# Optimization experiments

Hardware: AMD Instinct MI355X
Metric: run time of the kernel (lower is better)

## Reference

```python
import jax, jax.numpy as jnp
import numpy as np

B, T, N, K, d = 16, 64, 256, 8, 8
D = K * d
NEG = -9e15  # matches torch's -9000000000000000.0 sentinel


def _xavier(key, out_dim, in_dim):
    lim = float(np.sqrt(6.0 / (in_dim + out_dim)))
    return jax.random.uniform(key, (out_dim, in_dim), jnp.float32, -lim, lim)


def setup_inputs() -> dict:
    key = jax.random.key(0)
    ks = jax.random.split(key, 12)
    X = jax.random.normal(ks[0], (B, T, N, D), jnp.float32)
    STE = jax.random.normal(ks[1], (B, T, N, D), jnp.float32)
    W12 = _xavier(ks[2], D, 2 * D); b12 = jnp.zeros((D,), jnp.float32)
    W13 = _xavier(ks[3], D, 2 * D); b13 = jnp.zeros((D,), jnp.float32)
    W14 = _xavier(ks[4], D, 2 * D); b14 = jnp.zeros((D,), jnp.float32)
    W15 = _xavier(ks[5], D, D);     b15 = jnp.zeros((D,), jnp.float32)
    W16 = _xavier(ks[6], D, D);     b16 = jnp.zeros((D,), jnp.float32)
    return dict(X=X, STE=STE, W12=W12, b12=b12, W13=W13, b13=b13,
                W14=W14, b14=b14, W15=W15, b15=b15, W16=W16, b16=b16)


def reference(X, STE, W12, b12, W13, b13, W14, b14, W15, b15, W16, b16):
    gelu = lambda x: jax.nn.gelu(x, approximate=False)  # torch F.gelu default = erf
    Bv, Tv, Nv, Dv = X.shape
    H = jnp.concatenate([X, STE], axis=-1)              # [B,T,N,2D]
    # GELU-activated QKV projections, split into K heads of width d on last dim
    q = gelu(H @ W12.T + b12).reshape(Bv, Tv, Nv, K, d)
    k = gelu(H @ W13.T + b13).reshape(Bv, Tv, Nv, K, d)
    v = gelu(H @ W14.T + b14).reshape(Bv, Tv, Nv, K, d)
    # attention over time axis per (batch, vertex, head)
    attn = jnp.einsum('bqnkd,bsnkd->bnkqs', q, k) / jnp.sqrt(jnp.float32(d))
    causal = jnp.tril(jnp.ones((Tv, Tv), bool))         # [T,T]
    attn = jnp.where(causal, attn, jnp.float32(NEG))
    attn = jax.nn.softmax(attn, axis=-1)
    out = jnp.einsum('bnkqs,bsnkd->bqnkd', attn, v).reshape(Bv, Tv, Nv, Dv)
    # output MLP (dropout is identity in eval)
    return gelu(out @ W15.T + b15) @ W16.T + b16
```

## Files before the change

### kernel.cpp

```cpp
#include <hip/hip_runtime.h>
#include <hip/hip_bf16.h>

#define Bn 16
#define Tn 64
#define Nn 256
#define Kn 8
#define dn 8
#define Dn 64
#define TDn 128

typedef __bf16 bf16x8 __attribute__((ext_vector_type(8)));
typedef __bf16 bf16x4 __attribute__((ext_vector_type(4)));
typedef __bf16 bf16x2 __attribute__((ext_vector_type(2)));
typedef float  f32x4  __attribute__((ext_vector_type(4)));

#if __has_builtin(__builtin_amdgcn_exp2f)
#define EXP2F(x) __builtin_amdgcn_exp2f(x)
#else
#define EXP2F(x) exp2f(x)
#endif

#if __has_builtin(__builtin_amdgcn_rcpf)
#define RCPF(x) __builtin_amdgcn_rcpf(x)
#else
#define RCPF(x) (1.0f / (x))
#endif

__device__ __forceinline__ float geluf(float x) {
    const float x2 = x * x;
    const float v = x * fmaf(0.10294342f, x2, 2.30220920f);
    const float w = EXP2F(-fabsf(v));
    const float r = RCPF(1.0f + w);
    const float t = (1.0f - w) * r;
    return fmaf(0.5f * fabsf(x), t, 0.5f * x);
}

__device__ __forceinline__ bf16x8 bzero8() {
    bf16x8 z;
    #pragma unroll
    for (int e = 0; e < 8; ++e) z[e] = (__bf16)0.0f;
    return z;
}
__device__ __forceinline__ bf16x4 bzero4() {
    bf16x4 z;
    #pragma unroll
    for (int e = 0; e < 4; ++e) z[e] = (__bf16)0.0f;
    return z;
}

__global__ void convert_weights(const float* __restrict__ W12, const float* __restrict__ W13,
                                const float* __restrict__ W14, const float* __restrict__ W15,
                                const float* __restrict__ W16, __bf16* __restrict__ ws)
{
    const int i = blockIdx.x * 256 + threadIdx.x;
    float v;
    if      (i < 8192)  v = W12[i];
    else if (i < 16384) v = W13[i - 8192];
    else if (i < 24576) v = W14[i - 16384];
    else if (i < 28672) v = W15[i - 24576];
    else                v = W16[i - 28672];
    ws[i] = (__bf16)v;
}

template <int J>
__device__ __forceinline__ void attn_tile(__bf16 (*qs)[72], __bf16 (*Ps)[40],
                                          bf16x8 kf0, bf16x8 kf1, bf16x8 kf2, bf16x8 kf3,
                                          bf16x8 vf0, bf16x8 vf1,
                                          int hc, int cl, int quad, int kb)
{
    bf16x8 qf = bzero8();
    if (quad == 0) qf = *reinterpret_cast<const bf16x8*>(&qs[16 * J + cl][hc]);

    const f32x4 zc = {0.f, 0.f, 0.f, 0.f};
    f32x4 st[4];
    st[0] = __builtin_amdgcn_mfma_f32_16x16x32_bf16(kf0, qf, zc, 0, 0, 0);
    if constexpr (J >= 1) st[1] = __builtin_amdgcn_mfma_f32_16x16x32_bf16(kf1, qf, zc, 0, 0, 0);
    if constexpr (J >= 2) st[2] = __builtin_amdgcn_mfma_f32_16x16x32_bf16(kf2, qf, zc, 0, 0, 0);
    if constexpr (J >= 3) st[3] = __builtin_amdgcn_mfma_f32_16x16x32_bf16(kf3, qf, zc, 0, 0, 0);

    #pragma unroll
    for (int r = 0; r < 4; ++r)
        st[J][r] = (4 * quad + r > cl) ? -3.0e38f : st[J][r];

    float mx = -3.0e38f;
    #pragma unroll
    for (int i = 0; i <= J; ++i) {
        #pragma unroll
        for (int r = 0; r < 4; ++r) mx = fmaxf(mx, st[i][r]);
    }
    mx = fmaxf(mx, __shfl_xor(mx, 16));
    mx = fmaxf(mx, __shfl_xor(mx, 32));

    float sum = 0.f;
    #pragma unroll
    for (int i = 0; i <= J; ++i) {
        #pragma unroll
        for (int r = 0; r < 4; ++r) {
            const float p = EXP2F(st[i][r] - mx);
            st[i][r] = p;
            sum += p;
        }
    }
    sum += __shfl_xor(sum, 16);
    sum += __shfl_xor(sum, 32);

    f32x4 o = {0.f, 0.f, 0.f, 0.f};

    {
        bf16x4 pk0;
        #pragma unroll
        for (int r = 0; r < 4; ++r) pk0[r] = (__bf16)st[0][r];
        *reinterpret_cast<bf16x4*>(&Ps[cl][4 * quad]) = pk0;
        if constexpr (J >= 1) {
            bf16x4 pk1;
            #pragma unroll
            for (int r = 0; r < 4; ++r) pk1[r] = (__bf16)st[1][r];
            *reinterpret_cast<bf16x4*>(&Ps[cl][16 + 4 * quad]) = pk1;
        } else {
            *reinterpret_cast<bf16x4*>(&Ps[cl][16 + 4 * quad]) = bzero4();
        }
        const bf16x8 pf = *reinterpret_cast<const bf16x8*>(&Ps[cl][kb]);
        o = __builtin_amdgcn_mfma_f32_16x16x32_bf16(vf0, pf, o, 0, 0, 0);
    }
    if constexpr (J >= 2) {
        bf16x4 pk2;
        #pragma unroll
        for (int r = 0; r < 4; ++r) pk2[r] = (__bf16)st[2][r];
        *reinterpret_cast<bf16x4*>(&Ps[cl][4 * quad]) = pk2;
        if constexpr (J >= 3) {
            bf16x4 pk3;
            #pragma unroll
            for (int r = 0; r < 4; ++r) pk3[r] = (__bf16)st[3][r];
            *reinterpret_cast<bf16x4*>(&Ps[cl][16 + 4 * quad]) = pk3;
        } else {
            *reinterpret_cast<bf16x4*>(&Ps[cl][16 + 4 * quad]) = bzero4();
        }
        const bf16x8 pf = *reinterpret_cast<const bf16x8*>(&Ps[cl][kb]);
        o = __builtin_amdgcn_mfma_f32_16x16x32_bf16(vf1, pf, o, 0, 0, 0);
    }

    const float inv = RCPF(sum);
    if (quad < 2) {
        bf16x4 ov;
        #pragma unroll
        for (int r = 0; r < 4; ++r) ov[r] = (__bf16)(o[r] * inv);
        *reinterpret_cast<bf16x4*>(&qs[16 * J + cl][hc + 4 * quad]) = ov;
    }
}

__global__ __launch_bounds__(256, 5)
void tam_fused(const float* __restrict__ X,
               const float* __restrict__ STE,
               const float* __restrict__ b12, const float* __restrict__ b13,
               const float* __restrict__ b14, const float* __restrict__ b15,
               const float* __restrict__ b16,
               const __bf16* __restrict__ Wb,
               float* __restrict__ Out)
{
    __shared__ __align__(16) char smem[32768];
    __bf16 (*vt)[72] = reinterpret_cast<__bf16 (*)[72]>(smem);
    __bf16 (*qs)[72] = reinterpret_cast<__bf16 (*)[72]>(smem + 9216);
    __bf16 (*ks)[72] = reinterpret_cast<__bf16 (*)[72]>(smem + 18432);

    const int bn   = blockIdx.x;
    const int b    = bn >> 8;
    const int n    = bn & 255;
    const int tid  = threadIdx.x;
    const int lane = tid & 63;
    const int wv   = __builtin_amdgcn_readfirstlane(tid >> 6);
    const int cl   = lane & 15;
    const int quad = lane >> 4;
    const int kb   = quad * 8;
    const int m0   = wv * 16;

    __bf16 (*Ps)[40] = reinterpret_cast<__bf16 (*)[40]>(smem + 27648 + wv * 1280);

    const __bf16* Wqkv = Wb;
    const __bf16* W15b = Wb + 24576;
    const __bf16* W16b = Wb + 28672;

    {
        bf16x8 af[4];
        {
            const int t = m0 + cl;
            const size_t rb = (((size_t)b * Tn + t) * Nn + n) * (size_t)Dn;
            const float4* Xr = reinterpret_cast<const float4*>(X + rb);
            const float4* Sr = reinterpret_cast<const float4*>(STE + rb);
            #pragma unroll
            for (int kk = 0; kk < 4; ++kk) {
                const float4* src = (kk < 2) ? Xr : Sr;
                const int fi = (kk & 1) * 8 + quad * 2;
                const float4 f0 = src[fi];
                const float4 f1 = src[fi + 1];
                bf16x8 a;
                a[0] = (__bf16)f0.x; a[1] = (__bf16)f0.y;
                a[2] = (__bf16)f0.z; a[3] = (__bf16)f0.w;
                a[4] = (__bf16)f1.x; a[5] = (__bf16)f1.y;
                a[6] = (__bf16)f1.z; a[7] = (__bf16)f1.w;
                af[kk] = a;
            }
        }

        #pragma unroll
        for (int nt = 0; nt < 12; ++nt) {
            const int n0 = nt * 16;
            f32x4 acc = {0.f, 0.f, 0.f, 0.f};
            if (nt < 8) {
                #pragma unroll
                for (int kk = 0; kk < 4; ++kk) {
                    const bf16x8 bf = *reinterpret_cast<const bf16x8*>(
                        &Wqkv[(n0 + cl) * TDn + kk * 32 + kb]);
                    acc = __builtin_amdgcn_mfma_f32_16x16x32_bf16(bf, af[kk], acc, 0, 0, 0);
                }
                if (nt < 4) {
                    const float4 bs = *reinterpret_cast<const float4*>(&b12[n0 + 4 * quad]);
                    bf16x4 pk;
                    pk[0] = (__bf16)(geluf(acc[0] + bs.x) * 0.51006951f);
                    pk[1] = (__bf16)(geluf(acc[1] + bs.y) * 0.51006951f);
                    pk[2] = (__bf16)(geluf(acc[2] + bs.z) * 0.51006951f);
                    pk[3] = (__bf16)(geluf(acc[3] + bs.w) * 0.51006951f);
                    *reinterpret_cast<bf16x4*>(&qs[m0 + cl][n0 + 4 * quad]) = pk;
                } else {
                    const float4 bs = *reinterpret_cast<const float4*>(&b13[n0 - 64 + 4 * quad]);
                    bf16x4 pk;
                    pk[0] = (__bf16)geluf(acc[0] + bs.x);
                    pk[1] = (__bf16)geluf(acc[1] + bs.y);
                    pk[2] = (__bf16)geluf(acc[2] + bs.z);
                    pk[3] = (__bf16)geluf(acc[3] + bs.w);
                    *reinterpret_cast<bf16x4*>(&ks[m0 + cl][n0 - 64 + 4 * quad]) = pk;
                }
            } else {
                #pragma unroll
                for (int kk = 0; kk < 4; ++kk) {
                    const bf16x8 bf = *reinterpret_cast<const bf16x8*>(
                        &Wqkv[(n0 + cl) * TDn + kk * 32 + kb]);
                    acc = __builtin_amdgcn_mfma_f32_16x16x32_bf16(af[kk], bf, acc, 0, 0, 0);
                }
                const float bias = b14[n0 - 128 + cl];
                bf16x4 pv;
                #pragma unroll
                for (int r = 0; r < 4; ++r) pv[r] = (__bf16)geluf(acc[r] + bias);
                *reinterpret_cast<bf16x4*>(&vt[n0 - 128 + cl][m0 + 4 * quad]) = pv;
            }
        }
    }
    __syncthreads();

    {
        #pragma unroll
        for (int hh = 0; hh < 2; ++hh) {
            const int h  = 2 * wv + hh;
            const int hc = 8 * h;

            bf16x8 kf0 = bzero8(), kf1 = bzero8(), kf2 = bzero8(), kf3 = bzero8();
            if (quad == 0) {
                kf0 = *reinterpret_cast<const bf16x8*>(&ks[ 0 + cl][hc]);
                kf1 = *reinterpret_cast<const bf16x8*>(&ks[16 + cl][hc]);
                kf2 = *reinterpret_cast<const bf16x8*>(&ks[32 + cl][hc]);
                kf3 = *reinterpret_cast<const bf16x8*>(&ks[48 + cl][hc]);
            }
            bf16x8 vf0 = bzero8(), vf1 = bzero8();
            if (cl < 8) {
                vf0 = *reinterpret_cast<const bf16x8*>(&vt[hc + cl][kb]);
                vf1 = *reinterpret_cast<const bf16x8*>(&vt[hc + cl][32 + kb]);
            }

            attn_tile<0>(qs, Ps, kf0, kf1, kf2, kf3, vf0, vf1, hc, cl, quad, kb);
            attn_tile<1>(qs, Ps, kf0, kf1, kf2, kf3, vf0, vf1, hc, cl, quad, kb);
            attn_tile<2>(qs, Ps, kf0, kf1, kf2, kf3, vf0, vf1, hc, cl, quad, kb);
            attn_tile<3>(qs, Ps, kf0, kf1, kf2, kf3, vf0, vf1, hc, cl, quad, kb);
        }
    }
    __syncthreads();

    {
        const bf16x8 h0 = *reinterpret_cast<const bf16x8*>(&qs[m0 + cl][kb]);
        const bf16x8 h1 = *reinterpret_cast<const bf16x8*>(&qs[m0 + cl][32 + kb]);
        #pragma unroll
        for (int nt = 0; nt < 4; ++nt) {
            const int n0 = nt * 16;
            f32x4 acc = {0.f, 0.f, 0.f, 0.f};
            const bf16x8 w0 = *reinterpret_cast<const bf16x8*>(&W15b[(n0 + cl) * Dn + kb]);
            acc = __builtin_amdgcn_mfma_f32_16x16x32_bf16(w0, h0, acc, 0, 0, 0);
            const bf16x8 w1 = *reinterpret_cast<const bf16x8*>(&W15b[(n0 + cl) * Dn + 32 + kb]);
            acc = __builtin_amdgcn_mfma_f32_16x16x32_bf16(w1, h1, acc, 0, 0, 0);
            const float4 bs = *reinterpret_cast<const float4*>(&b15[n0 + 4 * quad]);
            bf16x4 pk;
            pk[0] = (__bf16)geluf(acc[0] + bs.x);
            pk[1] = (__bf16)geluf(acc[1] + bs.y);
            pk[2] = (__bf16)geluf(acc[2] + bs.z);
            pk[3] = (__bf16)geluf(acc[3] + bs.w);
            *reinterpret_cast<bf16x4*>(&ks[m0 + cl][n0 + 4 * quad]) = pk;
        }
    }

    {
        const bf16x8 h0 = *reinterpret_cast<const bf16x8*>(&ks[m0 + cl][kb]);
        const bf16x8 h1 = *reinterpret_cast<const bf16x8*>(&ks[m0 + cl][32 + kb]);
        const size_t ob = (((size_t)(b * Tn + m0 + cl)) * Nn + n) * (size_t)Dn;
        #pragma unroll
        for (int nt = 0; nt < 4; ++nt) {
            const int n0 = nt * 16;
            f32x4 acc = {0.f, 0.f, 0.f, 0.f};
            const bf16x8 w0 = *reinterpret_cast<const bf16x8*>(&W16b[(n0 + cl) * Dn + kb]);
            acc = __builtin_amdgcn_mfma_f32_16x16x32_bf16(w0, h0, acc, 0, 0, 0);
            const bf16x8 w1 = *reinterpret_cast<const bf16x8*>(&W16b[(n0 + cl) * Dn + 32 + kb]);
            acc = __builtin_amdgcn_mfma_f32_16x16x32_bf16(w1, h1, acc, 0, 0, 0);
            const float4 bs = *reinterpret_cast<const float4*>(&b16[n0 + 4 * quad]);
            float4 ov;
            ov.x = acc[0] + bs.x;
            ov.y = acc[1] + bs.y;
            ov.z = acc[2] + bs.z;
            ov.w = acc[3] + bs.w;
            *reinterpret_cast<float4*>(&Out[ob + n0 + 4 * quad]) = ov;
        }
    }
}

extern "C" void kernel_launch(void* const* d_in, const int* in_sizes, int n_in,
                              void* d_out, int out_size, void* d_ws, size_t ws_size,
                              hipStream_t stream)
{
    (void)in_sizes; (void)n_in; (void)out_size; (void)ws_size;
    const float* X   = (const float*)d_in[0];
    const float* STE = (const float*)d_in[1];
    const float* W12 = (const float*)d_in[2];
    const float* b12 = (const float*)d_in[3];
    const float* W13 = (const float*)d_in[4];
    const float* b13 = (const float*)d_in[5];
    const float* W14 = (const float*)d_in[6];
    const float* b14 = (const float*)d_in[7];
    const float* W15 = (const float*)d_in[8];
    const float* b15 = (const float*)d_in[9];
    const float* W16 = (const float*)d_in[10];
    const float* b16 = (const float*)d_in[11];
    float* Out = (float*)d_out;
    __bf16* ws = (__bf16*)d_ws;

    hipLaunchKernelGGL(convert_weights, dim3(128), dim3(256), 0, stream,
                       W12, W13, W14, W15, W16, ws);
    hipLaunchKernelGGL(tam_fused, dim3(Bn * Nn), dim3(256), 0, stream,
                       X, STE, b12, b13, b14, b15, b16, ws, Out);
}
```

Baseline: 282.0 us.

## Rewrite causal attention with 32x32 MFMA tiles and register shuffles for P

Replaces the four 16x16 query-tile attention steps with two 32x32x16 MFMA query tiles per head. The softmax probabilities are repacked into the B operand with cross-half lane shuffles instead of round-tripping through per-wave LDS scratch, which shrinks shared memory. The aim is fewer MFMA issues, no LDS traffic for P, and possibly higher occupancy. The cost is more registers for 16-wide accumulators and more wasted work on masked causal entries within the larger tiles.

```diff
diff --git a/kernel.cpp b/kernel.cpp
--- a/kernel.cpp
+++ b/kernel.cpp
@@ -13,6 +13,7 @@
 typedef __bf16 bf16x4 __attribute__((ext_vector_type(4)));
 typedef __bf16 bf16x2 __attribute__((ext_vector_type(2)));
 typedef float  f32x4  __attribute__((ext_vector_type(4)));
+typedef float  f32x16 __attribute__((ext_vector_type(16)));
 
 #if __has_builtin(__builtin_amdgcn_exp2f)
 #define EXP2F(x) __builtin_amdgcn_exp2f(x)
@@ -39,12 +40,6 @@
     bf16x8 z;
     #pragma unroll
     for (int e = 0; e < 8; ++e) z[e] = (__bf16)0.0f;
-    return z;
-}
-__device__ __forceinline__ bf16x4 bzero4() {
-    bf16x4 z;
-    #pragma unroll
-    for (int e = 0; e < 4; ++e) z[e] = (__bf16)0.0f;
     return z;
 }
 
@@ -62,92 +57,6 @@
     ws[i] = (__bf16)v;
 }
 
-template <int J>
-__device__ __forceinline__ void attn_tile(__bf16 (*qs)[72], __bf16 (*Ps)[40],
-                                          bf16x8 kf0, bf16x8 kf1, bf16x8 kf2, bf16x8 kf3,
-                                          bf16x8 vf0, bf16x8 vf1,
-                                          int hc, int cl, int quad, int kb)
-{
-    bf16x8 qf = bzero8();
-    if (quad == 0) qf = *reinterpret_cast<const bf16x8*>(&qs[16 * J + cl][hc]);
-
-    const f32x4 zc = {0.f, 0.f, 0.f, 0.f};
-    f32x4 st[4];
-    st[0] = __builtin_amdgcn_mfma_f32_16x16x32_bf16(kf0, qf, zc, 0, 0, 0);
-    if constexpr (J >= 1) st[1] = __builtin_amdgcn_mfma_f32_16x16x32_bf16(kf1, qf, zc, 0, 0, 0);
-    if constexpr (J >= 2) st[2] = __builtin_amdgcn_mfma_f32_16x16x32_bf16(kf2, qf, zc, 0, 0, 0);
-    if constexpr (J >= 3) st[3] = __builtin_amdgcn_mfma_f32_16x16x32_bf16(kf3, qf, zc, 0, 0, 0);
-
-    #pragma unroll
-    for (int r = 0; r < 4; ++r)
-        st[J][r] = (4 * quad + r > cl) ? -3.0e38f : st[J][r];
-
-    float mx = -3.0e38f;
-    #pragma unroll
-    for (int i = 0; i <= J; ++i) {
-        #pragma unroll
-        for (int r = 0; r < 4; ++r) mx = fmaxf(mx, st[i][r]);
-    }
-    mx = fmaxf(mx, __shfl_xor(mx, 16));
-    mx = fmaxf(mx, __shfl_xor(mx, 32));
-
-    float sum = 0.f;
-    #pragma unroll
-    for (int i = 0; i <= J; ++i) {
-        #pragma unroll
-        for (int r = 0; r < 4; ++r) {
-            const float p = EXP2F(st[i][r] - mx);
-            st[i][r] = p;
-            sum += p;
-        }
-    }
-    sum += __shfl_xor(sum, 16);
-    sum += __shfl_xor(sum, 32);
-
-    f32x4 o = {0.f, 0.f, 0.f, 0.f};
-
-    {
-        bf16x4 pk0;
-        #pragma unroll
-        for (int r = 0; r < 4; ++r) pk0[r] = (__bf16)st[0][r];
-        *reinterpret_cast<bf16x4*>(&Ps[cl][4 * quad]) = pk0;
-        if constexpr (J >= 1) {
-            bf16x4 pk1;
-            #pragma unroll
-            for (int r = 0; r < 4; ++r) pk1[r] = (__bf16)st[1][r];
-            *reinterpret_cast<bf16x4*>(&Ps[cl][16 + 4 * quad]) = pk1;
-        } else {
-            *reinterpret_cast<bf16x4*>(&Ps[cl][16 + 4 * quad]) = bzero4();
-        }
-        const bf16x8 pf = *reinterpret_cast<const bf16x8*>(&Ps[cl][kb]);
-        o = __builtin_amdgcn_mfma_f32_16x16x32_bf16(vf0, pf, o, 0, 0, 0);
-    }
-    if constexpr (J >= 2) {
-        bf16x4 pk2;
-        #pragma unroll
-        for (int r = 0; r < 4; ++r) pk2[r] = (__bf16)st[2][r];
-        *reinterpret_cast<bf16x4*>(&Ps[cl][4 * quad]) = pk2;
-        if constexpr (J >= 3) {
-            bf16x4 pk3;
-            #pragma unroll
-            for (int r = 0; r < 4; ++r) pk3[r] = (__bf16)st[3][r];
-            *reinterpret_cast<bf16x4*>(&Ps[cl][16 + 4 * quad]) = pk3;
-        } else {
-            *reinterpret_cast<bf16x4*>(&Ps[cl][16 + 4 * quad]) = bzero4();
-        }
-        const bf16x8 pf = *reinterpret_cast<const bf16x8*>(&Ps[cl][kb]);
-        o = __builtin_amdgcn_mfma_f32_16x16x32_bf16(vf1, pf, o, 0, 0, 0);
-    }
-
-    const float inv = RCPF(sum);
-    if (quad < 2) {
-        bf16x4 ov;
-        #pragma unroll
-        for (int r = 0; r < 4; ++r) ov[r] = (__bf16)(o[r] * inv);
-        *reinterpret_cast<bf16x4*>(&qs[16 * J + cl][hc + 4 * quad]) = ov;
-    }
-}
-
 __global__ __launch_bounds__(256, 5)
 void tam_fused(const float* __restrict__ X,
                const float* __restrict__ STE,
@@ -157,7 +66,7 @@
                const __bf16* __restrict__ Wb,
                float* __restrict__ Out)
 {
-    __shared__ __align__(16) char smem[32768];
+    __shared__ __align__(16) char smem[27648];
     __bf16 (*vt)[72] = reinterpret_cast<__bf16 (*)[72]>(smem);
     __bf16 (*qs)[72] = reinterpret_cast<__bf16 (*)[72]>(smem + 9216);
     __bf16 (*ks)[72] = reinterpret_cast<__bf16 (*)[72]>(smem + 18432);
@@ -172,8 +81,6 @@
     const int quad = lane >> 4;
     const int kb   = quad * 8;
     const int m0   = wv * 16;
-
-    __bf16 (*Ps)[40] = reinterpret_cast<__bf16 (*)[40]>(smem + 27648 + wv * 1280);
 
     const __bf16* Wqkv = Wb;
     const __bf16* W15b = Wb + 24576;
@@ -247,28 +154,132 @@
     __syncthreads();
 
     {
-        #pragma unroll
+        const int half = lane >> 5;
+        const int l31  = lane & 31;
+
         for (int hh = 0; hh < 2; ++hh) {
-            const int h  = 2 * wv + hh;
-            const int hc = 8 * h;
-
-            bf16x8 kf0 = bzero8(), kf1 = bzero8(), kf2 = bzero8(), kf3 = bzero8();
-            if (quad == 0) {
-                kf0 = *reinterpret_cast<const bf16x8*>(&ks[ 0 + cl][hc]);
-                kf1 = *reinterpret_cast<const bf16x8*>(&ks[16 + cl][hc]);
-                kf2 = *reinterpret_cast<const bf16x8*>(&ks[32 + cl][hc]);
-                kf3 = *reinterpret_cast<const bf16x8*>(&ks[48 + cl][hc]);
-            }
-            bf16x8 vf0 = bzero8(), vf1 = bzero8();
-            if (cl < 8) {
-                vf0 = *reinterpret_cast<const bf16x8*>(&vt[hc + cl][kb]);
-                vf1 = *reinterpret_cast<const bf16x8*>(&vt[hc + cl][32 + kb]);
-            }
-
-            attn_tile<0>(qs, Ps, kf0, kf1, kf2, kf3, vf0, vf1, hc, cl, quad, kb);
-            attn_tile<1>(qs, Ps, kf0, kf1, kf2, kf3, vf0, vf1, hc, cl, quad, kb);
-            attn_tile<2>(qs, Ps, kf0, kf1, kf2, kf3, vf0, vf1, hc, cl, quad, kb);
-            attn_tile<3>(qs, Ps, kf0, kf1, kf2, kf3, vf0, vf1, hc, cl, quad, kb);
+            const int hc = 8 * (2 * wv + hh);
+
+            bf16x8 kA0 = bzero8(), kA1 = bzero8(), qB0 = bzero8(), qB1 = bzero8();
+            if (half == 0) {
+                kA0 = *reinterpret_cast<const bf16x8*>(&ks[ 0 + l31][hc]);
+                kA1 = *reinterpret_cast<const bf16x8*>(&ks[32 + l31][hc]);
+                qB0 = *reinterpret_cast<const bf16x8*>(&qs[ 0 + l31][hc]);
+                qB1 = *reinterpret_cast<const bf16x8*>(&qs[32 + l31][hc]);
+            }
+            bf16x8 vA0 = bzero8(), vA1 = bzero8(), vA2 = bzero8(), vA3 = bzero8();
+            if (l31 < 8) {
+                vA0 = *reinterpret_cast<const bf16x8*>(&vt[hc + l31][ 0 + 8 * half]);
+                vA1 = *reinterpret_cast<const bf16x8*>(&vt[hc + l31][16 + 8 * half]);
+                vA2 = *reinterpret_cast<const bf16x8*>(&vt[hc + l31][32 + 8 * half]);
+                vA3 = *reinterpret_cast<const bf16x8*>(&vt[hc + l31][48 + 8 * half]);
+            }
+
+            f32x16 zc16;
+            #pragma unroll
+            for (int r = 0; r < 16; ++r) zc16[r] = 0.f;
+
+            {
+                f32x16 S = __builtin_amdgcn_mfma_f32_32x32x16_bf16(kA0, qB0, zc16, 0, 0, 0);
+                #pragma unroll
+                for (int r = 0; r < 16; ++r) {
+                    const int tk = (r & 3) + 8 * (r >> 2) + 4 * half;
+                    S[r] = (tk > l31) ? -3.0e38f : S[r];
+                }
+                float mx = S[0];
+                #pragma unroll
+                for (int r = 1; r < 16; ++r) mx = fmaxf(mx, S[r]);
+                mx = fmaxf(mx, __shfl_xor(mx, 32));
+                float sum = 0.f;
+                #pragma unroll
+                for (int r = 0; r < 16; ++r) { const float p = EXP2F(S[r] - mx); S[r] = p; sum += p; }
+                sum += __shfl_xor(sum, 32);
+
+                unsigned u[8];
+                #pragma unroll
+                for (int i = 0; i < 8; ++i) {
+                    union { __bf16 h[2]; unsigned w; } cv;
+                    cv.h[0] = (__bf16)S[2 * i]; cv.h[1] = (__bf16)S[2 * i + 1];
+                    u[i] = cv.w;
+                }
+                f32x16 O = zc16;
+                #pragma unroll
+                for (int c = 0; c < 2; ++c) {
+                    const unsigned x0 = __shfl_xor(u[4 * c + 0], 32);
+                    const unsigned x1 = __shfl_xor(u[4 * c + 1], 32);
+                    const unsigned x2 = __shfl_xor(u[4 * c + 2], 32);
+                    const unsigned x3 = __shfl_xor(u[4 * c + 3], 32);
+                    union { unsigned w[4]; bf16x8 v; } bw;
+                    bw.w[0] = half ? x2 : u[4 * c + 0];
+                    bw.w[1] = half ? x3 : u[4 * c + 1];
+                    bw.w[2] = half ? u[4 * c + 2] : x0;
+                    bw.w[3] = half ? u[4 * c + 3] : x1;
+                    O = __builtin_amdgcn_mfma_f32_32x32x16_bf16(c ? vA1 : vA0, bw.v, O, 0, 0, 0);
+                }
+                const float inv = RCPF(sum);
+                bf16x4 ov;
+                #pragma unroll
+                for (int r = 0; r < 4; ++r) ov[r] = (__bf16)(O[r] * inv);
+                *reinterpret_cast<bf16x4*>(&qs[l31][hc + 4 * half]) = ov;
+            }
+
+            {
+                f32x16 Sa = __builtin_amdgcn_mfma_f32_32x32x16_bf16(kA0, qB1, zc16, 0, 0, 0);
+                f32x16 Sb = __builtin_amdgcn_mfma_f32_32x32x16_bf16(kA1, qB1, zc16, 0, 0, 0);
+                #pragma unroll
+                for (int r = 0; r < 16; ++r) {
+                    const int tk = (r & 3) + 8 * (r >> 2) + 4 * half;
+                    Sb[r] = (tk > l31) ? -3.0e38f : Sb[r];
+                }
+                float mx = Sa[0];
+                #pragma unroll
+                for (int r = 1; r < 16; ++r) mx = fmaxf(mx, Sa[r]);
+                #pragma unroll
+                for (int r = 0; r < 16; ++r) mx = fmaxf(mx, Sb[r]);
+                mx = fmaxf(mx, __shfl_xor(mx, 32));
+                float sum = 0.f;
+                #pragma unroll
+                for (int r = 0; r < 16; ++r) { const float p = EXP2F(Sa[r] - mx); Sa[r] = p; sum += p; }
+                #pragma unroll
+                for (int r = 0; r < 16; ++r) { const float p = EXP2F(Sb[r] - mx); Sb[r] = p; sum += p; }
+                sum += __shfl_xor(sum, 32);
+
+                unsigned ua[8], ub[8];
+                #pragma unroll
+                for (int i = 0; i < 8; ++i) {
+                    union { __bf16 h[2]; unsigned w; } cv;
+                    cv.h[0] = (__bf16)Sa[2 * i]; cv.h[1] = (__bf16)Sa[2 * i + 1];
+                    ua[i] = cv.w;
+                }
+                #pragma unroll
+                for (int i = 0; i < 8; ++i) {
+                    union { __bf16 h[2]; unsigned w; } cv;
+                    cv.h[0] = (__bf16)Sb[2 * i]; cv.h[1] = (__bf16)Sb[2 * i + 1];
+                    ub[i] = cv.w;
+                }
+                f32x16 O = zc16;
+                #pragma unroll
+                for (int c = 0; c < 4; ++c) {
+                    const unsigned* uu = (c < 2) ? ua : ub;
+                    const int c2 = c & 1;
+                    const unsigned x0 = __shfl_xor(uu[4 * c2 + 0], 32);
+                    const unsigned x1 = __shfl_xor(uu[4 * c2 + 1], 32);
+                    const unsigned x2 = __shfl_xor(uu[4 * c2 + 2], 32);
+                    const unsigned x3 = __shfl_xor(uu[4 * c2 + 3], 32);
+                    union { unsigned w[4]; bf16x8 v; } bw;
+                    bw.w[0] = half ? x2 : uu[4 * c2 + 0];
+                    bw.w[1] = half ? x3 : uu[4 * c2 + 1];
+                    bw.w[2] = half ? uu[4 * c2 + 2] : x0;
+                    bw.w[3] = half ? uu[4 * c2 + 3] : x1;
+                    const bf16x8 vA = (c == 0) ? vA0 : (c == 1) ? vA1 : (c == 2) ? vA2 : vA3;
+                    O = __builtin_amdgcn_mfma_f32_32x32x16_bf16(vA, bw.v, O, 0, 0, 0);
+                }
+                const float inv = RCPF(sum);
+                bf16x4 ov;
+                #pragma unroll
+                for (int r = 0; r < 4; ++r) ov[r] = (__bf16)(O[r] * inv);
+                *reinterpret_cast<bf16x4*>(&qs[32 + l31][hc + 4 * half]) = ov;
+            }
         }
     }
     __syncthreads();
```

New measurement: 281.9 us. No clear change (-0.0%).
